# Kernel tuning notes

Hardware: AMD Instinct MI355X
Metric: run time of the kernel (lower is better)

The kernel has to match this reference:

```python
import jax, jax.numpy as jnp
import numpy as np

N, E, HID, LAT = 50000, 800000, 128, 64
IN_NODE, IN_EDGE, NL = 11, 4, 2


def setup_inputs() -> dict:
    key = jax.random.key(0)
    ks = jax.random.split(key, 16)
    def rn(k, shape, scale=0.05):
        return jax.random.normal(k, shape, dtype=jnp.float32) * scale
    return {
        "h0": jax.random.normal(ks[0], (N, IN_NODE), jnp.float32),
        "label": jax.random.normal(ks[1], (N, 7), jnp.float32),
        "x": jax.random.normal(ks[2], (N, 3), jnp.float32),
        "edge_attr": jax.random.normal(ks[3], (E, IN_EDGE), jnp.float32),
        "eps": jax.random.normal(ks[4], (N, LAT), jnp.float32),
        "emb_w": rn(ks[5], (IN_NODE, HID)),
        "emb_b": jnp.zeros((HID,), jnp.float32),
        "edge_w1": rn(ks[6], (NL, 2 * HID + 1 + IN_EDGE, HID)),
        "edge_b1": jnp.zeros((NL, HID), jnp.float32),
        "edge_w2": rn(ks[7], (NL, HID, HID)),
        "edge_b2": jnp.zeros((NL, HID), jnp.float32),
        "node_w1": rn(ks[8], (NL, 3 * HID, HID)),
        "node_b1": jnp.zeros((NL, HID), jnp.float32),
        "node_w2": rn(ks[9], (NL, HID, HID)),
        "node_b2": jnp.zeros((NL, HID), jnp.float32),
        "mu_w": rn(ks[10], (HID + 7, LAT)),
        "mu_b": jnp.zeros((LAT,), jnp.float32),
        "var_w": rn(ks[11], (HID + 7, LAT)),
        "var_b": jnp.zeros((LAT,), jnp.float32),
        "edges": jax.random.randint(ks[12], (2, E), 0, N, dtype=jnp.int32),
        "n_nodes": N,
    }


def reference(h0, label, x, edge_attr, eps, emb_w, emb_b, edge_w1, edge_b1,
              edge_w2, edge_b2, node_w1, node_b1, node_w2, node_b2,
              mu_w, mu_b, var_w, var_b, edges, n_nodes):
    elu = jax.nn.elu
    row, col = edges[0], edges[1]
    # coord2radial: squared distance per edge [E,1]
    coord_diff = x[row] - x[col]
    radial = jnp.sum(coord_diff * coord_diff, axis=1, keepdims=True)
    # node embedding
    h = h0 @ emb_w + emb_b
    for i in range(NL):
        # edge_model: gather endpoints, fuse through 2-layer ELU MLP
        ef = jnp.concatenate([h[row], h[col], radial, edge_attr], axis=1)  # [E, 2H+1+IN_EDGE]
        ef = elu(ef @ edge_w1[i] + edge_b1[i])
        ef = elu(ef @ edge_w2[i] + edge_b2[i])
        # node_model: scatter-sum messages to source nodes, node_attr = h
        agg = jax.ops.segment_sum(ef, row, num_segments=n_nodes)  # [N, H]
        nf = jnp.concatenate([h, agg, h], axis=1)  # [N, 3H]
        nf = elu(nf @ node_w1[i] + node_b1[i])
        h = nf @ node_w2[i] + node_b2[i]  # recurrent=False: no residual
    hl = jnp.concatenate([h, label], axis=1)  # [N, H+7]
    mu = hl @ mu_w + mu_b
    log_var = hl @ var_w + var_b
    std = jnp.exp(log_var * 0.5)
    z = mu + 0.01 * eps * std
    return z
```

## Files before the change

kernel.cpp:

```cpp
#include <hip/hip_runtime.h>
#include <hip/hip_bf16.h>
#include <math.h>

#define N_NODES 50000
#define N_EDGES 800000
#define HID 128
#define LAT 64
#define IN_NODE 11
#define K_EDGE 261
#define KP1 288
#define KN 256
#define KO 160
#define AST 296
#define NST 264
#define TST 136
#define MST 132
#define HLST 168
#define OST 132
#define TE 32
#define NTPB 20
#define NTN 2
#define NSCAN 196
#define EB 3125
#define EMB_B 25000
#define WPB 32
#define ZB 100

typedef __attribute__((ext_vector_type(8))) short short8;
typedef __attribute__((ext_vector_type(4))) short short4v;
typedef __attribute__((ext_vector_type(4))) float floatx4;

__device__ __forceinline__ float elu_f(float v) { return v > 0.0f ? v : __expf(v) - 1.0f; }

__device__ __forceinline__ short f2bf(float f) {
    unsigned int u = __builtin_bit_cast(unsigned int, f);
    u += 0x7fffu + ((u >> 16) & 1u);
    return (short)(u >> 16);
}

__device__ __forceinline__ short2 f2bf2(float a, float b) {
    float2 p; p.x = a; p.y = b;
    __hip_bfloat162 h = __float22bfloat162_rn(p);
    short2 r;
    __builtin_memcpy(&r, &h, sizeof(r));
    return r;
}

__device__ __forceinline__ float bf2f(short s) {
    unsigned int u = ((unsigned int)(unsigned short)s) << 16;
    return __builtin_bit_cast(float, u);
}

__global__ void prep_all(const int* __restrict__ edges, const float* __restrict__ h0,
                         const float* __restrict__ emb_w, const float* __restrict__ emb_b,
                         const float* __restrict__ ew1, const float* __restrict__ ew2,
                         const float* __restrict__ nw1, const float* __restrict__ nw2,
                         const float* __restrict__ mu_w, const float* __restrict__ mu_b,
                         const float* __restrict__ var_w, const float* __restrict__ var_b,
                         int* __restrict__ cnt,
                         short* __restrict__ h_bf,
                         short* __restrict__ ew1T, short* __restrict__ ew2T,
                         short* __restrict__ nw1T, short* __restrict__ nw2T,
                         short* __restrict__ owT,
                         float* __restrict__ agg) {
    int b = blockIdx.x, t = threadIdx.x;
    if (b < EB) {
        int e = b * 256 + t;
        if (e >= N_EDGES) return;
        atomicAdd(&cnt[edges[e]], 1);
    } else if (b < EB + EMB_B) {
        int bb = b - EB;
        int n = bb * 2 + (t >> 7);
        int c = t & 127;
        if (n >= N_NODES) return;
        float acc = emb_b[c];
        #pragma unroll
        for (int k = 0; k < IN_NODE; ++k) acc += h0[n*IN_NODE + k] * emb_w[k*HID + c];
        h_bf[(size_t)n*HID + c] = f2bf(acc);
    } else if (b < EB + EMB_B + WPB) {
        int idx = (b - EB - EMB_B) * 256 + t;
        int stride = WPB * 256;
        for (int i = idx; i < 2*128*KP1; i += stride) {
            int l = i / (128*KP1); int r = i % (128*KP1);
            int c = r / KP1; int k = r % KP1;
            float v = (k < K_EDGE) ? ew1[(size_t)l*K_EDGE*128 + (size_t)k*128 + c] : 0.0f;
            ew1T[i] = f2bf(v);
        }
        for (int i = idx; i < 2*128*128; i += stride) {
            int l = i / (128*128); int r = i % (128*128);
            int c = r / 128; int k = r % 128;
            ew2T[i] = f2bf(ew2[(size_t)l*128*128 + (size_t)k*128 + c]);
        }
        for (int i = idx; i < 2*128*KN; i += stride) {
            int l = i / (128*KN); int r = i % (128*KN);
            int c = r / KN; int k = r % KN;
            const float* base = nw1 + (size_t)l*384*128;
            float v = (k < 128) ? (base[(size_t)k*128 + c] + base[(size_t)(256+k)*128 + c])
                                : base[(size_t)k*128 + c];
            nw1T[i] = f2bf(v);
        }
        for (int i = idx; i < 2*128*128; i += stride) {
            int l = i / (128*128); int r = i % (128*128);
            int c = r / 128; int k = r % 128;
            nw2T[i] = f2bf(nw2[(size_t)l*128*128 + (size_t)k*128 + c]);
        }
        for (int i = idx; i < 128*KO; i += stride) {
            int c = i / KO; int k = i % KO;
            float v = 0.0f;
            if (c < 64) {
                if (k < 135) v = mu_w[(size_t)k*LAT + c];
                else if (k == 135) v = mu_b[c];
            } else {
                int cc = c - 64;
                if (k < 135) v = var_w[(size_t)k*LAT + cc];
                else if (k == 135) v = var_b[cc];
            }
            owT[i] = f2bf(v);
        }
    } else {
        int idx = (b - EB - EMB_B - WPB) * 256 + t;
        int stride = ZB * 256;
        float4 z = {0,0,0,0};
        float4* a4 = (float4*)agg;
        for (int i = idx; i < N_NODES*HID/4; i += stride) a4[i] = z;
    }
}

__global__ void scan_a(const int* __restrict__ cnt, int* __restrict__ cursor,
                       int* __restrict__ blk) {
    __shared__ int s[256];
    int b = blockIdx.x, t = threadIdx.x;
    int row = b * 256 + t;
    int v = (row < N_NODES) ? cnt[row] : 0;
    s[t] = v;
    __syncthreads();
    #pragma unroll
    for (int off = 1; off < 256; off <<= 1) {
        int add = (t >= off) ? s[t - off] : 0;
        __syncthreads();
        s[t] += add;
        __syncthreads();
    }
    if (row < N_NODES) cursor[row] = s[t] - v;
    if (t == 255) blk[b] = s[255];
}

__global__ void scan_b(int* __restrict__ blk) {
    __shared__ int s[256];
    int t = threadIdx.x;
    int v = (t < NSCAN) ? blk[t] : 0;
    s[t] = v;
    __syncthreads();
    #pragma unroll
    for (int off = 1; off < 256; off <<= 1) {
        int add = (t >= off) ? s[t - off] : 0;
        __syncthreads();
        s[t] += add;
        __syncthreads();
    }
    if (t < NSCAN) blk[t] = s[t] - v;
}

__global__ void csr_place(const int* __restrict__ edges, const float* __restrict__ x,
                          const float* __restrict__ edge_attr,
                          int* __restrict__ cursor, const int* __restrict__ blk,
                          int* __restrict__ srow, int* __restrict__ scol,
                          short* __restrict__ tail_s) {
    int e = blockIdx.x * 256 + threadIdx.x;
    if (e >= N_EDGES) return;
    int r = edges[e], c = edges[N_EDGES + e];
    float dx = x[r*3+0] - x[c*3+0];
    float dy = x[r*3+1] - x[c*3+1];
    float dz = x[r*3+2] - x[c*3+2];
    float radial = dx*dx + dy*dy + dz*dz;
    float4 ea = *(const float4*)(edge_attr + (size_t)e * 4);
    short8 s = { f2bf(radial), f2bf(ea.x), f2bf(ea.y), f2bf(ea.z), f2bf(ea.w), 0, 0, 0 };
    int pos = atomicAdd(&cursor[r], 1) + blk[r >> 8];
    srow[pos] = r; scol[pos] = c;
    *(short8*)(tail_s + (size_t)pos * 8) = s;
}

__global__ __launch_bounds__(256, 2) void edge_mfma_kernel(
    const short* __restrict__ h_bf, const short* __restrict__ tail_s,
    const int* __restrict__ srow, const int* __restrict__ scol,
    const short* __restrict__ w1T, const float* __restrict__ b1,
    const short* __restrict__ w2T, const float* __restrict__ b2,
    float* __restrict__ agg)
{
    __shared__ __align__(16) short featA[TE * AST];
    __shared__ __align__(16) short t1[TE * TST];
    __shared__ int srowS[TE];
    float* msgF = (float*)featA;
    int t = threadIdx.x;
    int lane = t & 63;
    int wv = t >> 6;
    int l15 = lane & 15;
    int quad = lane >> 4;
    int el = t >> 3, j = t & 7;

    short8 aw1[2][9], aw2[2][4];
    float4 b1v[2], b2v[2];
    #pragma unroll
    for (int mi = 0; mi < 2; ++mi) {
        #pragma unroll
        for (int ks = 0; ks < 9; ++ks)
            aw1[mi][ks] = *(const short8*)&w1T[(size_t)(wv*32 + mi*16 + l15)*KP1 + ks*32 + quad*8];
        #pragma unroll
        for (int ks = 0; ks < 4; ++ks)
            aw2[mi][ks] = *(const short8*)&w2T[(size_t)(wv*32 + mi*16 + l15)*128 + ks*32 + quad*8];
        b1v[mi] = *(const float4*)&b1[wv*32 + mi*16 + quad*4];
        b2v[mi] = *(const float4*)&b2[wv*32 + mi*16 + quad*4];
    }

    for (int it = 0; it < NTPB; ++it) {
        int e0 = (blockIdx.x * NTPB + it) * TE;
        __syncthreads();

        {
            int e = e0 + el;
            int r = srow[e], c = scol[e];
            if (j == 0) srowS[el] = r;
            const short8* hr = (const short8*)(h_bf + (size_t)r * HID + j*16);
            const short8* hc = (const short8*)(h_bf + (size_t)c * HID + j*16);
            short8 s0 = hr[0], s1 = hr[1];
            short8 s2 = hc[0], s3 = hc[1];
            *(short8*)&featA[el*AST + j*16]       = s0;
            *(short8*)&featA[el*AST + j*16 + 8]   = s1;
            *(short8*)&featA[el*AST + 128 + j*16]     = s2;
            *(short8*)&featA[el*AST + 128 + j*16 + 8] = s3;
        }
        if (t < TE) {
            int e = e0 + t;
            short8 s = *(const short8*)(tail_s + (size_t)e * 8);
            short8 z = {0,0,0,0,0,0,0,0};
            *(short8*)&featA[t*AST + 256] = s;
            *(short8*)&featA[t*AST + 264] = z;
            *(short8*)&featA[t*AST + 272] = z;
            *(short8*)&featA[t*AST + 280] = z;
        }
        __syncthreads();

        floatx4 acc[2][2] = {{{0,0,0,0},{0,0,0,0}},{{0,0,0,0},{0,0,0,0}}};
        #pragma unroll
        for (int ks = 0; ks < 9; ++ks) {
            int koff = ks*32 + quad*8;
            short8 bb0 = *(const short8*)&featA[l15*AST + koff];
            short8 bb1 = *(const short8*)&featA[(16 + l15)*AST + koff];
            acc[0][0] = __builtin_amdgcn_mfma_f32_16x16x32_bf16(aw1[0][ks], bb0, acc[0][0], 0, 0, 0);
            acc[0][1] = __builtin_amdgcn_mfma_f32_16x16x32_bf16(aw1[0][ks], bb1, acc[0][1], 0, 0, 0);
            acc[1][0] = __builtin_amdgcn_mfma_f32_16x16x32_bf16(aw1[1][ks], bb0, acc[1][0], 0, 0, 0);
            acc[1][1] = __builtin_amdgcn_mfma_f32_16x16x32_bf16(aw1[1][ks], bb1, acc[1][1], 0, 0, 0);
        }

        #pragma unroll
        for (int mi = 0; mi < 2; ++mi) {
            int cb = wv*32 + mi*16 + quad*4;
            #pragma unroll
            for (int ni = 0; ni < 2; ++ni) {
                short2 q0 = f2bf2(elu_f(acc[mi][ni][0] + b1v[mi].x),
                                  elu_f(acc[mi][ni][1] + b1v[mi].y));
                short2 q1 = f2bf2(elu_f(acc[mi][ni][2] + b1v[mi].z),
                                  elu_f(acc[mi][ni][3] + b1v[mi].w));
                short4v s = { q0.x, q0.y, q1.x, q1.y };
                *(short4v*)&t1[(ni*16 + l15)*TST + cb] = s;
            }
        }
        __syncthreads();

        floatx4 acc2[2][2] = {{{0,0,0,0},{0,0,0,0}},{{0,0,0,0},{0,0,0,0}}};
        #pragma unroll
        for (int ks = 0; ks < 4; ++ks) {
            int koff = ks*32 + quad*8;
            short8 bb0 = *(const short8*)&t1[l15*TST + koff];
            short8 bb1 = *(const short8*)&t1[(16 + l15)*TST + koff];
            acc2[0][0] = __builtin_amdgcn_mfma_f32_16x16x32_bf16(aw2[0][ks], bb0, acc2[0][0], 0, 0, 0);
            acc2[0][1] = __builtin_amdgcn_mfma_f32_16x16x32_bf16(aw2[0][ks], bb1, acc2[0][1], 0, 0, 0);
            acc2[1][0] = __builtin_amdgcn_mfma_f32_16x16x32_bf16(aw2[1][ks], bb0, acc2[1][0], 0, 0, 0);
            acc2[1][1] = __builtin_amdgcn_mfma_f32_16x16x32_bf16(aw2[1][ks], bb1, acc2[1][1], 0, 0, 0);
        }

        #pragma unroll
        for (int mi = 0; mi < 2; ++mi) {
            int cb = wv*32 + mi*16 + quad*4;
            #pragma unroll
            for (int ni = 0; ni < 2; ++ni) {
                float4 v = { elu_f(acc2[mi][ni][0] + b2v[mi].x), elu_f(acc2[mi][ni][1] + b2v[mi].y),
                             elu_f(acc2[mi][ni][2] + b2v[mi].z), elu_f(acc2[mi][ni][3] + b2v[mi].w) };
                *(float4*)&msgF[(ni*16 + l15)*MST + cb] = v;
            }
        }
        __syncthreads();

        {
            int ch = t & 127, half = t >> 7;
            int base = half * 16;
            int prow = srowS[base];
            float run = 0.0f;
            #pragma unroll
            for (int i = 0; i < 16; ++i) {
                int rr = srowS[base + i];
                if (rr != prow) {
                    unsafeAtomicAdd(&agg[(size_t)prow * HID + ch], run);
                    run = 0.0f; prow = rr;
                }
                run += msgF[(base + i)*MST + ch];
            }
            unsafeAtomicAdd(&agg[(size_t)prow * HID + ch], run);
        }
    }
}

__global__ __launch_bounds__(256, 2) void node_mfma_kernel(
    const short* __restrict__ h_bf, float* __restrict__ agg,
    const short* __restrict__ w1T, const float* __restrict__ b1,
    const short* __restrict__ w2T, const float* __restrict__ b2,
    const short* __restrict__ owT, const float* __restrict__ label,
    const float* __restrict__ eps, float* __restrict__ zout,
    short* __restrict__ hout_bf, int zero_agg, int do_out)
{
    __shared__ __align__(16) short featN[32 * NST];
    __shared__ __align__(16) short t1[32 * TST];
    __shared__ __align__(16) short hlB[32 * HLST];
    float* outB = (float*)featN;
    int t = threadIdx.x;
    int lane = t & 63;
    int wv = t >> 6;
    int l15 = lane & 15;
    int quad = lane >> 4;
    int nl = t >> 3, j = t & 7;

    short8 aw1[2][8], aw2[2][4];
    float4 b1v[2], b2v[2];
    #pragma unroll
    for (int mi = 0; mi < 2; ++mi) {
        #pragma unroll
        for (int ks = 0; ks < 8; ++ks)
            aw1[mi][ks] = *(const short8*)&w1T[(size_t)(wv*32 + mi*16 + l15)*KN + ks*32 + quad*8];
        #pragma unroll
        for (int ks = 0; ks < 4; ++ks)
            aw2[mi][ks] = *(const short8*)&w2T[(size_t)(wv*32 + mi*16 + l15)*128 + ks*32 + quad*8];
        b1v[mi] = *(const float4*)&b1[wv*32 + mi*16 + quad*4];
        b2v[mi] = *(const float4*)&b2[wv*32 + mi*16 + quad*4];
    }

    for (int it = 0; it < NTN; ++it) {
        int n0 = (blockIdx.x * NTN + it) * 32;
        if (n0 >= N_NODES) break;
        __syncthreads();

        int n = n0 + nl;
        int idx = n < N_NODES ? n : N_NODES - 1;
        {
            const short8* hp = (const short8*)(h_bf + (size_t)idx * HID + j*16);
            short8 s0 = hp[0], s1 = hp[1];
            const float4* ap = (const float4*)(agg + (size_t)idx * HID) + j*4;
            float4 u0 = ap[0], u1 = ap[1], u2 = ap[2], u3 = ap[3];
            short2 p0 = f2bf2(u0.x, u0.y), p1 = f2bf2(u0.z, u0.w);
            short2 p2 = f2bf2(u1.x, u1.y), p3 = f2bf2(u1.z, u1.w);
            short2 p4 = f2bf2(u2.x, u2.y), p5 = f2bf2(u2.z, u2.w);
            short2 p6 = f2bf2(u3.x, u3.y), p7 = f2bf2(u3.z, u3.w);
            short8 s2 = { p0.x, p0.y, p1.x, p1.y, p2.x, p2.y, p3.x, p3.y };
            short8 s3 = { p4.x, p4.y, p5.x, p5.y, p6.x, p6.y, p7.x, p7.y };
            *(short8*)&featN[nl*NST + j*16]       = s0;
            *(short8*)&featN[nl*NST + j*16 + 8]   = s1;
            *(short8*)&featN[nl*NST + 128 + j*16]     = s2;
            *(short8*)&featN[nl*NST + 128 + j*16 + 8] = s3;
        }
        __syncthreads();

        if (zero_agg && n < N_NODES) {
            float4 z = {0,0,0,0};
            float4* ap = (float4*)(agg + (size_t)n * HID) + j*4;
            ap[0] = z; ap[1] = z; ap[2] = z; ap[3] = z;
        }

        floatx4 acc[2][2] = {{{0,0,0,0},{0,0,0,0}},{{0,0,0,0},{0,0,0,0}}};
        #pragma unroll
        for (int ks = 0; ks < 8; ++ks) {
            int koff = ks*32 + quad*8;
            short8 bb0 = *(const short8*)&featN[l15*NST + koff];
            short8 bb1 = *(const short8*)&featN[(16 + l15)*NST + koff];
            acc[0][0] = __builtin_amdgcn_mfma_f32_16x16x32_bf16(aw1[0][ks], bb0, acc[0][0], 0, 0, 0);
            acc[0][1] = __builtin_amdgcn_mfma_f32_16x16x32_bf16(aw1[0][ks], bb1, acc[0][1], 0, 0, 0);
            acc[1][0] = __builtin_amdgcn_mfma_f32_16x16x32_bf16(aw1[1][ks], bb0, acc[1][0], 0, 0, 0);
            acc[1][1] = __builtin_amdgcn_mfma_f32_16x16x32_bf16(aw1[1][ks], bb1, acc[1][1], 0, 0, 0);
        }

        #pragma unroll
        for (int mi = 0; mi < 2; ++mi) {
            int cb = wv*32 + mi*16 + quad*4;
            #pragma unroll
            for (int ni = 0; ni < 2; ++ni) {
                short2 p0 = f2bf2(elu_f(acc[mi][ni][0] + b1v[mi].x),
                                  elu_f(acc[mi][ni][1] + b1v[mi].y));
                short2 p1 = f2bf2(elu_f(acc[mi][ni][2] + b1v[mi].z),
                                  elu_f(acc[mi][ni][3] + b1v[mi].w));
                short4v s = { p0.x, p0.y, p1.x, p1.y };
                *(short4v*)&t1[(ni*16 + l15)*TST + cb] = s;
            }
        }
        __syncthreads();

        floatx4 acc2[2][2] = {{{0,0,0,0},{0,0,0,0}},{{0,0,0,0},{0,0,0,0}}};
        #pragma unroll
        for (int ks = 0; ks < 4; ++ks) {
            int koff = ks*32 + quad*8;
            short8 bb0 = *(const short8*)&t1[l15*TST + koff];
            short8 bb1 = *(const short8*)&t1[(16 + l15)*TST + koff];
            acc2[0][0] = __builtin_amdgcn_mfma_f32_16x16x32_bf16(aw2[0][ks], bb0, acc2[0][0], 0, 0, 0);
            acc2[0][1] = __builtin_amdgcn_mfma_f32_16x16x32_bf16(aw2[0][ks], bb1, acc2[0][1], 0, 0, 0);
            acc2[1][0] = __builtin_amdgcn_mfma_f32_16x16x32_bf16(aw2[1][ks], bb0, acc2[1][0], 0, 0, 0);
            acc2[1][1] = __builtin_amdgcn_mfma_f32_16x16x32_bf16(aw2[1][ks], bb1, acc2[1][1], 0, 0, 0);
        }

        if (!do_out) {
            #pragma unroll
            for (int mi = 0; mi < 2; ++mi) {
                int cb = wv*32 + mi*16 + quad*4;
                #pragma unroll
                for (int ni = 0; ni < 2; ++ni) {
                    int nn = n0 + ni*16 + l15;
                    if (nn < N_NODES) {
                        short2 p0 = f2bf2(acc2[mi][ni][0] + b2v[mi].x, acc2[mi][ni][1] + b2v[mi].y);
                        short2 p1 = f2bf2(acc2[mi][ni][2] + b2v[mi].z, acc2[mi][ni][3] + b2v[mi].w);
                        short4v s = { p0.x, p0.y, p1.x, p1.y };
                        *(short4v*)&hout_bf[(size_t)nn*HID + cb] = s;
                    }
                }
            }
        } else {
            #pragma unroll
            for (int mi = 0; mi < 2; ++mi) {
                int cb = wv*32 + mi*16 + quad*4;
                #pragma unroll
                for (int ni = 0; ni < 2; ++ni) {
                    short2 p0 = f2bf2(acc2[mi][ni][0] + b2v[mi].x, acc2[mi][ni][1] + b2v[mi].y);
                    short2 p1 = f2bf2(acc2[mi][ni][2] + b2v[mi].z, acc2[mi][ni][3] + b2v[mi].w);
                    short4v s = { p0.x, p0.y, p1.x, p1.y };
                    *(short4v*)&hlB[(ni*16 + l15)*HLST + cb] = s;
                }
            }
            if (t < 32) {
                int nn = n0 + t;
                int ii = nn < N_NODES ? nn : N_NODES - 1;
                const float* lp = label + (size_t)ii * 7;
                short8 s = { f2bf(lp[0]), f2bf(lp[1]), f2bf(lp[2]), f2bf(lp[3]),
                             f2bf(lp[4]), f2bf(lp[5]), f2bf(lp[6]), f2bf(1.0f) };
                short8 z = {0,0,0,0,0,0,0,0};
                *(short8*)&hlB[t*HLST + 128] = s;
                *(short8*)&hlB[t*HLST + 136] = z;
                *(short8*)&hlB[t*HLST + 144] = z;
                *(short8*)&hlB[t*HLST + 152] = z;
            }
            __syncthreads();

            floatx4 accO[2][2] = {{{0,0,0,0},{0,0,0,0}},{{0,0,0,0},{0,0,0,0}}};
            short8 awO[2][5];
            #pragma unroll
            for (int mi = 0; mi < 2; ++mi)
                #pragma unroll
                for (int ks = 0; ks < 5; ++ks)
                    awO[mi][ks] = *(const short8*)&owT[(size_t)(wv*32 + mi*16 + l15)*KO + ks*32 + quad*8];
            #pragma unroll
            for (int ks = 0; ks < 5; ++ks) {
                int koff = ks*32 + quad*8;
                short8 bb0 = *(const short8*)&hlB[l15*HLST + koff];
                short8 bb1 = *(const short8*)&hlB[(16 + l15)*HLST + koff];
                accO[0][0] = __builtin_amdgcn_mfma_f32_16x16x32_bf16(awO[0][ks], bb0, accO[0][0], 0, 0, 0);
                accO[0][1] = __builtin_amdgcn_mfma_f32_16x16x32_bf16(awO[0][ks], bb1, accO[0][1], 0, 0, 0);
                accO[1][0] = __builtin_amdgcn_mfma_f32_16x16x32_bf16(awO[1][ks], bb0, accO[1][0], 0, 0, 0);
                accO[1][1] = __builtin_amdgcn_mfma_f32_16x16x32_bf16(awO[1][ks], bb1, accO[1][1], 0, 0, 0);
            }
            #pragma unroll
            for (int mi = 0; mi < 2; ++mi) {
                int cg = wv*32 + mi*16 + quad*4;
                #pragma unroll
                for (int ni = 0; ni < 2; ++ni) {
                    float4 v = { accO[mi][ni][0], accO[mi][ni][1], accO[mi][ni][2], accO[mi][ni][3] };
                    *(float4*)&outB[(ni*16 + l15)*OST + cg] = v;
                }
            }
            __syncthreads();

            {
                int c = t & 63, g = t >> 6;
                #pragma unroll
                for (int i = 0; i < 8; ++i) {
                    int nloc = g*8 + i;
                    int nn = n0 + nloc;
                    if (nn < N_NODES) {
                        float mu = outB[nloc*OST + c];
                        float va = outB[nloc*OST + 64 + c];
                        zout[(size_t)nn*LAT + c] = mu + 0.01f * eps[(size_t)nn*LAT + c] * __expf(va * 0.5f);
                    }
                }
            }
        }
    }
}

extern "C" void kernel_launch(void* const* d_in, const int* in_sizes, int n_in,
                              void* d_out, int out_size, void* d_ws, size_t ws_size,
                              hipStream_t stream) {
    const float* h0        = (const float*)d_in[0];
    const float* label     = (const float*)d_in[1];
    const float* x         = (const float*)d_in[2];
    const float* edge_attr = (const float*)d_in[3];
    const float* eps       = (const float*)d_in[4];
    const float* emb_w     = (const float*)d_in[5];
    const float* emb_b     = (const float*)d_in[6];
    const float* edge_w1   = (const float*)d_in[7];
    const float* edge_b1   = (const float*)d_in[8];
    const float* edge_w2   = (const float*)d_in[9];
    const float* edge_b2   = (const float*)d_in[10];
    const float* node_w1   = (const float*)d_in[11];
    const float* node_b1   = (const float*)d_in[12];
    const float* node_w2   = (const float*)d_in[13];
    const float* node_b2   = (const float*)d_in[14];
    const float* mu_w      = (const float*)d_in[15];
    const float* mu_b      = (const float*)d_in[16];
    const float* var_w     = (const float*)d_in[17];
    const float* var_b     = (const float*)d_in[18];
    const int*   edges     = (const int*)d_in[19];
    float* out = (float*)d_out;

    float* agg      = (float*)d_ws;
    short* h_bf     = (short*)(agg + (size_t)N_NODES * HID);
    short* tail_s   = h_bf + (size_t)N_NODES * HID;
    int*   cnt      = (int*)(tail_s + (size_t)N_EDGES * 8);
    int*   cursor   = cnt + N_NODES;
    int*   blk      = cursor + N_NODES;
    int*   srow     = blk + 256;
    int*   scol     = srow + N_EDGES;
    short* ew1T     = (short*)(scol + N_EDGES);
    short* ew2T     = ew1T + 2*128*KP1;
    short* nw1T     = ew2T + 2*128*128;
    short* nw2T     = nw1T + 2*128*KN;
    short* owT      = nw2T + 2*128*128;

    hipMemsetAsync(cnt, 0, N_NODES * sizeof(int), stream);
    prep_all<<<EB + EMB_B + WPB + ZB, 256, 0, stream>>>(
        edges, h0, emb_w, emb_b,
        edge_w1, edge_w2, node_w1, node_w2,
        mu_w, mu_b, var_w, var_b,
        cnt, h_bf, ew1T, ew2T, nw1T, nw2T, owT, agg);
    scan_a<<<NSCAN, 256, 0, stream>>>(cnt, cursor, blk);
    scan_b<<<1, 256, 0, stream>>>(blk);
    csr_place<<<(N_EDGES + 255) / 256, 256, 0, stream>>>(edges, x, edge_attr, cursor, blk,
                                                         srow, scol, tail_s);

    for (int l = 0; l < 2; ++l) {
        edge_mfma_kernel<<<N_EDGES / TE / NTPB, 256, 0, stream>>>(
            h_bf, tail_s, srow, scol,
            ew1T + (size_t)l * 128 * KP1, edge_b1 + l * HID,
            ew2T + (size_t)l * 128 * 128, edge_b2 + l * HID, agg);
        node_mfma_kernel<<<(N_NODES/32 + NTN) / NTN, 256, 0, stream>>>(
            h_bf, agg,
            nw1T + (size_t)l * 128 * KN, node_b1 + l * HID,
            nw2T + (size_t)l * 128 * 128, node_b2 + l * HID,
            owT, label, eps, out, h_bf,
            (l == 0) ? 1 : 0, (l == 1) ? 1 : 0);
    }
}
```

Before: 612.7 us.

## Precompute per-node edge-MLP first-layer projections instead of per-edge GEMM

The first edge-MLP layer is split by linearity: each node's h is projected through the row and col halves of edge_w1 once per node (N work) and stored as a 256-wide fp32 table. Each edge then gathers two 128-float slices, adds them, and applies the small radial/edge_attr terms and bias in scalar code, replacing the per-edge 288-K MFMA. For layer 0 the embedding is folded into composed weights computed by a new small kernel. For layer 1 the node kernel appends an MFMA that writes the projection table. The aim is to cut edge-side compute, at the cost of gathering fp32 rows (twice the bytes of the bf16 gathers) and extra work in the node kernel.

Result: faster. 592.4 us (-3.3%).

```diff
diff --git a/kernel.cpp b/kernel.cpp
--- a/kernel.cpp
+++ b/kernel.cpp
@@ -7,11 +7,8 @@
 #define HID 128
 #define LAT 64
 #define IN_NODE 11
-#define K_EDGE 261
-#define KP1 288
 #define KN 256
 #define KO 160
-#define AST 296
 #define NST 264
 #define TST 136
 #define MST 132
@@ -51,17 +48,33 @@
     return __builtin_bit_cast(float, u);
 }
 
+__global__ void compose_k(const float* __restrict__ emb_w, const float* __restrict__ emb_b,
+                          const float* __restrict__ ew1, float* __restrict__ cw) {
+    int k0 = blockIdx.x;
+    int mm = threadIdx.x;
+    int m = mm & 127;
+    int base = (mm < 128) ? 0 : 128;
+    float s = 0.0f;
+    for (int k = 0; k < 128; ++k) {
+        float w = ew1[(size_t)(base + k) * 128 + m];
+        float e = (k0 < 11) ? emb_w[k0 * 128 + k] : emb_b[k];
+        s += e * w;
+    }
+    cw[k0 * 256 + mm] = s;
+}
+
 __global__ void prep_all(const int* __restrict__ edges, const float* __restrict__ h0,
                          const float* __restrict__ emb_w, const float* __restrict__ emb_b,
                          const float* __restrict__ ew1, const float* __restrict__ ew2,
                          const float* __restrict__ nw1, const float* __restrict__ nw2,
                          const float* __restrict__ mu_w, const float* __restrict__ mu_b,
                          const float* __restrict__ var_w, const float* __restrict__ var_b,
+                         const float* __restrict__ cw,
                          int* __restrict__ cnt,
-                         short* __restrict__ h_bf,
-                         short* __restrict__ ew1T, short* __restrict__ ew2T,
+                         short* __restrict__ h_bf, float* __restrict__ aG,
+                         short* __restrict__ ew2T,
                          short* __restrict__ nw1T, short* __restrict__ nw2T,
-                         short* __restrict__ owT,
+                         short* __restrict__ owT, short* __restrict__ awaT,
                          float* __restrict__ agg) {
     int b = blockIdx.x, t = threadIdx.x;
     if (b < EB) {
@@ -73,19 +86,24 @@
         int n = bb * 2 + (t >> 7);
         int c = t & 127;
         if (n >= N_NODES) return;
+        float h0v[IN_NODE];
+        #pragma unroll
+        for (int k = 0; k < IN_NODE; ++k) h0v[k] = h0[n*IN_NODE + k];
         float acc = emb_b[c];
         #pragma unroll
-        for (int k = 0; k < IN_NODE; ++k) acc += h0[n*IN_NODE + k] * emb_w[k*HID + c];
+        for (int k = 0; k < IN_NODE; ++k) acc += h0v[k] * emb_w[k*HID + c];
         h_bf[(size_t)n*HID + c] = f2bf(acc);
+        float s0 = cw[11*256 + c], s1 = cw[11*256 + 128 + c];
+        #pragma unroll
+        for (int k = 0; k < IN_NODE; ++k) {
+            s0 += h0v[k] * cw[k*256 + c];
+            s1 += h0v[k] * cw[k*256 + 128 + c];
+        }
+        aG[(size_t)n*256 + c]       = s0;
+        aG[(size_t)n*256 + 128 + c] = s1;
     } else if (b < EB + EMB_B + WPB) {
         int idx = (b - EB - EMB_B) * 256 + t;
         int stride = WPB * 256;
-        for (int i = idx; i < 2*128*KP1; i += stride) {
-            int l = i / (128*KP1); int r = i % (128*KP1);
-            int c = r / KP1; int k = r % KP1;
-            float v = (k < K_EDGE) ? ew1[(size_t)l*K_EDGE*128 + (size_t)k*128 + c] : 0.0f;
-            ew1T[i] = f2bf(v);
-        }
         for (int i = idx; i < 2*128*128; i += stride) {
             int l = i / (128*128); int r = i % (128*128);
             int c = r / 128; int k = r % 128;
@@ -116,6 +134,12 @@
                 else if (k == 135) v = var_b[cc];
             }
             owT[i] = f2bf(v);
+        }
+        for (int i = idx; i < 2*256*128; i += stride) {
+            int l = i / (256*128); int r = i % (256*128);
+            int mm = r / 128; int k = r % 128;
+            int kk = (mm < 128) ? k : 128 + k;
+            awaT[i] = f2bf(ew1[(size_t)l*261*128 + (size_t)kk*128 + (mm & 127)]);
         }
     } else {
         int idx = (b - EB - EMB_B - WPB) * 256 + t;
@@ -181,89 +205,73 @@
 }
 
 __global__ __launch_bounds__(256, 2) void edge_mfma_kernel(
-    const short* __restrict__ h_bf, const short* __restrict__ tail_s,
+    const float* __restrict__ aG, const short* __restrict__ tail_s,
     const int* __restrict__ srow, const int* __restrict__ scol,
-    const short* __restrict__ w1T, const float* __restrict__ b1,
+    const float* __restrict__ w1c, const float* __restrict__ b1,
     const short* __restrict__ w2T, const float* __restrict__ b2,
     float* __restrict__ agg)
 {
-    __shared__ __align__(16) short featA[TE * AST];
     __shared__ __align__(16) short t1[TE * TST];
-    __shared__ int srowS[TE];
-    float* msgF = (float*)featA;
+    __shared__ __align__(16) float msgF[TE * MST];
+    __shared__ int srowS[2][TE];
     int t = threadIdx.x;
     int lane = t & 63;
     int wv = t >> 6;
     int l15 = lane & 15;
     int quad = lane >> 4;
-    int el = t >> 3, j = t & 7;
-
-    short8 aw1[2][9], aw2[2][4];
-    float4 b1v[2], b2v[2];
+    int cg = t & 15;
+    int elb = t >> 4;
+
+    float w1cv[5][8];
+    float b1v8[8];
+    #pragma unroll
+    for (int k = 0; k < 5; ++k)
+        #pragma unroll
+        for (int j = 0; j < 8; ++j)
+            w1cv[k][j] = w1c[k*128 + cg*8 + j];
+    #pragma unroll
+    for (int j = 0; j < 8; ++j) b1v8[j] = b1[cg*8 + j];
+
+    short8 aw2[2][4];
+    float4 b2v[2];
     #pragma unroll
     for (int mi = 0; mi < 2; ++mi) {
         #pragma unroll
-        for (int ks = 0; ks < 9; ++ks)
-            aw1[mi][ks] = *(const short8*)&w1T[(size_t)(wv*32 + mi*16 + l15)*KP1 + ks*32 + quad*8];
-        #pragma unroll
         for (int ks = 0; ks < 4; ++ks)
             aw2[mi][ks] = *(const short8*)&w2T[(size_t)(wv*32 + mi*16 + l15)*128 + ks*32 + quad*8];
-        b1v[mi] = *(const float4*)&b1[wv*32 + mi*16 + quad*4];
         b2v[mi] = *(const float4*)&b2[wv*32 + mi*16 + quad*4];
     }
 
     for (int it = 0; it < NTPB; ++it) {
         int e0 = (blockIdx.x * NTPB + it) * TE;
-        __syncthreads();
-
-        {
+        int pb = it & 1;
+        if (t < TE) srowS[pb][t] = srow[e0 + t];
+
+        #pragma unroll
+        for (int ii = 0; ii < 2; ++ii) {
+            int el = elb + ii*16;
             int e = e0 + el;
             int r = srow[e], c = scol[e];
-            if (j == 0) srowS[el] = r;
-            const short8* hr = (const short8*)(h_bf + (size_t)r * HID + j*16);
-            const short8* hc = (const short8*)(h_bf + (size_t)c * HID + j*16);
-            short8 s0 = hr[0], s1 = hr[1];
-            short8 s2 = hc[0], s3 = hc[1];
-            *(short8*)&featA[el*AST + j*16]       = s0;
-            *(short8*)&featA[el*AST + j*16 + 8]   = s1;
-            *(short8*)&featA[el*AST + 128 + j*16]     = s2;
-            *(short8*)&featA[el*AST + 128 + j*16 + 8] = s3;
-        }
-        if (t < TE) {
-            int e = e0 + t;
-            short8 s = *(const short8*)(tail_s + (size_t)e * 8);
-            short8 z = {0,0,0,0,0,0,0,0};
-            *(short8*)&featA[t*AST + 256] = s;
-            *(short8*)&featA[t*AST + 264] = z;
-            *(short8*)&featA[t*AST + 272] = z;
-            *(short8*)&featA[t*AST + 280] = z;
-        }
-        __syncthreads();
-
-        floatx4 acc[2][2] = {{{0,0,0,0},{0,0,0,0}},{{0,0,0,0},{0,0,0,0}}};
-        #pragma unroll
-        for (int ks = 0; ks < 9; ++ks) {
-            int koff = ks*32 + quad*8;
-            short8 bb0 = *(const short8*)&featA[l15*AST + koff];
-            short8 bb1 = *(const short8*)&featA[(16 + l15)*AST + koff];
-            acc[0][0] = __builtin_amdgcn_mfma_f32_16x16x32_bf16(aw1[0][ks], bb0, acc[0][0], 0, 0, 0);
-            acc[0][1] = __builtin_amdgcn_mfma_f32_16x16x32_bf16(aw1[0][ks], bb1, acc[0][1], 0, 0, 0);
-            acc[1][0] = __builtin_amdgcn_mfma_f32_16x16x32_bf16(aw1[1][ks], bb0, acc[1][0], 0, 0, 0);
-            acc[1][1] = __builtin_amdgcn_mfma_f32_16x16x32_bf16(aw1[1][ks], bb1, acc[1][1], 0, 0, 0);
-        }
-
-        #pragma unroll
-        for (int mi = 0; mi < 2; ++mi) {
-            int cb = wv*32 + mi*16 + quad*4;
-            #pragma unroll
-            for (int ni = 0; ni < 2; ++ni) {
-                short2 q0 = f2bf2(elu_f(acc[mi][ni][0] + b1v[mi].x),
-                                  elu_f(acc[mi][ni][1] + b1v[mi].y));
-                short2 q1 = f2bf2(elu_f(acc[mi][ni][2] + b1v[mi].z),
-                                  elu_f(acc[mi][ni][3] + b1v[mi].w));
-                short4v s = { q0.x, q0.y, q1.x, q1.y };
-                *(short4v*)&t1[(ni*16 + l15)*TST + cb] = s;
-            }
+            const float4* p1 = (const float4*)(aG + (size_t)r * 256 + cg*8);
+            const float4* p2 = (const float4*)(aG + (size_t)c * 256 + 128 + cg*8);
+            float4 x0 = p1[0], x1 = p1[1];
+            float4 y0 = p2[0], y1 = p2[1];
+            short8 tl = *(const short8*)(tail_s + (size_t)e * 8);
+            float t0 = bf2f(tl[0]), t1f = bf2f(tl[1]), t2 = bf2f(tl[2]),
+                  t3 = bf2f(tl[3]), t4 = bf2f(tl[4]);
+            float s[8] = { x0.x+y0.x, x0.y+y0.y, x0.z+y0.z, x0.w+y0.w,
+                           x1.x+y1.x, x1.y+y1.y, x1.z+y1.z, x1.w+y1.w };
+            float v[8];
+            #pragma unroll
+            for (int j = 0; j < 8; ++j) {
+                v[j] = elu_f(s[j] + b1v8[j]
+                       + t0*w1cv[0][j] + t1f*w1cv[1][j] + t2*w1cv[2][j]
+                       + t3*w1cv[3][j] + t4*w1cv[4][j]);
+            }
+            short2 q0 = f2bf2(v[0], v[1]), q1 = f2bf2(v[2], v[3]);
+            short2 q2 = f2bf2(v[4], v[5]), q3 = f2bf2(v[6], v[7]);
+            short8 o = { q0.x, q0.y, q1.x, q1.y, q2.x, q2.y, q3.x, q3.y };
+            *(short8*)&t1[el*TST + cg*8] = o;
         }
         __syncthreads();
 
@@ -294,11 +302,11 @@
         {
             int ch = t & 127, half = t >> 7;
             int base = half * 16;
-            int prow = srowS[base];
+            int prow = srowS[pb][base];
             float run = 0.0f;
             #pragma unroll
             for (int i = 0; i < 16; ++i) {
-                int rr = srowS[base + i];
+                int rr = srowS[pb][base + i];
                 if (rr != prow) {
                     unsafeAtomicAdd(&agg[(size_t)prow * HID + ch], run);
                     run = 0.0f; prow = rr;
@@ -316,7 +324,8 @@
     const short* __restrict__ w2T, const float* __restrict__ b2,
     const short* __restrict__ owT, const float* __restrict__ label,
     const float* __restrict__ eps, float* __restrict__ zout,
-    short* __restrict__ hout_bf, int zero_agg, int do_out)
+    short* __restrict__ hout_bf, const short* __restrict__ awaT1,
+    float* __restrict__ aGout, int zero_agg, int do_out)
 {
     __shared__ __align__(16) short featN[32 * NST];
     __shared__ __align__(16) short t1[32 * TST];
@@ -414,17 +423,44 @@
         }
 
         if (!do_out) {
+            __syncthreads();
             #pragma unroll
             for (int mi = 0; mi < 2; ++mi) {
                 int cb = wv*32 + mi*16 + quad*4;
                 #pragma unroll
                 for (int ni = 0; ni < 2; ++ni) {
                     int nn = n0 + ni*16 + l15;
+                    short2 p0 = f2bf2(acc2[mi][ni][0] + b2v[mi].x, acc2[mi][ni][1] + b2v[mi].y);
+                    short2 p1 = f2bf2(acc2[mi][ni][2] + b2v[mi].z, acc2[mi][ni][3] + b2v[mi].w);
+                    short4v s = { p0.x, p0.y, p1.x, p1.y };
+                    if (nn < N_NODES) *(short4v*)&hout_bf[(size_t)nn*HID + cb] = s;
+                    *(short4v*)&t1[(ni*16 + l15)*TST + cb] = s;
+                }
+            }
+            __syncthreads();
+            floatx4 accA[4][2] = {{{0,0,0,0},{0,0,0,0}},{{0,0,0,0},{0,0,0,0}},
+                                  {{0,0,0,0},{0,0,0,0}},{{0,0,0,0},{0,0,0,0}}};
+            #pragma unroll
+            for (int ks = 0; ks < 4; ++ks) {
+                int koff = ks*32 + quad*8;
+                short8 bb0 = *(const short8*)&t1[l15*TST + koff];
+                short8 bb1 = *(const short8*)&t1[(16 + l15)*TST + koff];
+                #pragma unroll
+                for (int mi = 0; mi < 4; ++mi) {
+                    short8 wf = *(const short8*)&awaT1[(size_t)(wv*64 + mi*16 + l15)*128 + ks*32 + quad*8];
+                    accA[mi][0] = __builtin_amdgcn_mfma_f32_16x16x32_bf16(wf, bb0, accA[mi][0], 0, 0, 0);
+                    accA[mi][1] = __builtin_amdgcn_mfma_f32_16x16x32_bf16(wf, bb1, accA[mi][1], 0, 0, 0);
+                }
+            }
+            #pragma unroll
+            for (int mi = 0; mi < 4; ++mi) {
+                int mm = wv*64 + mi*16 + quad*4;
+                #pragma unroll
+                for (int ni = 0; ni < 2; ++ni) {
+                    int nn = n0 + ni*16 + l15;
                     if (nn < N_NODES) {
-                        short2 p0 = f2bf2(acc2[mi][ni][0] + b2v[mi].x, acc2[mi][ni][1] + b2v[mi].y);
-                        short2 p1 = f2bf2(acc2[mi][ni][2] + b2v[mi].z, acc2[mi][ni][3] + b2v[mi].w);
-                        short4v s = { p0.x, p0.y, p1.x, p1.y };
-                        *(short4v*)&hout_bf[(size_t)nn*HID + cb] = s;
+                        float4 v = { accA[mi][ni][0], accA[mi][ni][1], accA[mi][ni][2], accA[mi][ni][3] };
+                        *(float4*)&aGout[(size_t)nn*256 + mm] = v;
                     }
                 }
             }
@@ -473,11 +509,11 @@
             }
             #pragma unroll
             for (int mi = 0; mi < 2; ++mi) {
-                int cg = wv*32 + mi*16 + quad*4;
+                int cg2 = wv*32 + mi*16 + quad*4;
                 #pragma unroll
                 for (int ni = 0; ni < 2; ++ni) {
                     float4 v = { accO[mi][ni][0], accO[mi][ni][1], accO[mi][ni][2], accO[mi][ni][3] };
-                    *(float4*)&outB[(ni*16 + l15)*OST + cg] = v;
+                    *(float4*)&outB[(ni*16 + l15)*OST + cg2] = v;
                 }
             }
             __syncthreads();
@@ -525,25 +561,28 @@
     float* out = (float*)d_out;
 
     float* agg      = (float*)d_ws;
-    short* h_bf     = (short*)(agg + (size_t)N_NODES * HID);
+    float* aG       = agg + (size_t)N_NODES * HID;
+    short* h_bf     = (short*)(aG + (size_t)N_NODES * 256);
     short* tail_s   = h_bf + (size_t)N_NODES * HID;
     int*   cnt      = (int*)(tail_s + (size_t)N_EDGES * 8);
     int*   cursor   = cnt + N_NODES;
     int*   blk      = cursor + N_NODES;
     int*   srow     = blk + 256;
     int*   scol     = srow + N_EDGES;
-    short* ew1T     = (short*)(scol + N_EDGES);
-    short* ew2T     = ew1T + 2*128*KP1;
+    short* ew2T     = (short*)(scol + N_EDGES);
     short* nw1T     = ew2T + 2*128*128;
     short* nw2T     = nw1T + 2*128*KN;
     short* owT      = nw2T + 2*128*128;
+    short* awaT     = owT + 128*KO;
+    float* cw       = (float*)(awaT + 2*256*128);
 
     hipMemsetAsync(cnt, 0, N_NODES * sizeof(int), stream);
+    compose_k<<<12, 256, 0, stream>>>(emb_w, emb_b, edge_w1, cw);
     prep_all<<<EB + EMB_B + WPB + ZB, 256, 0, stream>>>(
         edges, h0, emb_w, emb_b,
         edge_w1, edge_w2, node_w1, node_w2,
-        mu_w, mu_b, var_w, var_b,
-        cnt, h_bf, ew1T, ew2T, nw1T, nw2T, owT, agg);
+        mu_w, mu_b, var_w, var_b, cw,
+        cnt, h_bf, aG, ew2T, nw1T, nw2T, owT, awaT, agg);
     scan_a<<<NSCAN, 256, 0, stream>>>(cnt, cursor, blk);
     scan_b<<<1, 256, 0, stream>>>(blk);
     csr_place<<<(N_EDGES + 255) / 256, 256, 0, stream>>>(edges, x, edge_attr, cursor, blk,
@@ -551,14 +590,15 @@
 
     for (int l = 0; l < 2; ++l) {
         edge_mfma_kernel<<<N_EDGES / TE / NTPB, 256, 0, stream>>>(
-            h_bf, tail_s, srow, scol,
-            ew1T + (size_t)l * 128 * KP1, edge_b1 + l * HID,
+            aG, tail_s, srow, scol,
+            edge_w1 + (size_t)l * 261 * 128 + 256 * 128, edge_b1 + l * HID,
             ew2T + (size_t)l * 128 * 128, edge_b2 + l * HID, agg);
         node_mfma_kernel<<<(N_NODES/32 + NTN) / NTN, 256, 0, stream>>>(
             h_bf, agg,
             nw1T + (size_t)l * 128 * KN, node_b1 + l * HID,
             nw2T + (size_t)l * 128 * 128, node_b2 + l * HID,
             owT, label, eps, out, h_bf,
+            awaT + 256 * 128, aG,
             (l == 0) ? 1 : 0, (l == 1) ? 1 : 0);
     }
 }
```
